# Kernel tuning notes

Hardware: AMD Instinct MI355X
Metric: run time of the kernel (lower is better)

Reference implementation:

```python
import jax, jax.numpy as jnp
import numpy as np

EPS = 1e-12
B, C, H, M, E, P = 2, 20000, 64, 8, 200000, 3


def setup_inputs() -> dict:
    key = jax.random.key(0)
    ks = jax.random.split(key, 24)
    inp = {}
    inp["features"] = jax.random.normal(ks[0], (B, C, H), jnp.float32)
    inp["positions"] = jax.random.normal(ks[1], (B, C, P), jnp.float32)
    inp["edge_index"] = jax.random.randint(ks[2], (2, E), 0, C)
    inp["degree"] = jax.random.randint(ks[3], (C,), 1, 33).astype(jnp.float32)
    inp["cell_node_indices"] = jax.random.randint(ks[4], (C, M), 0, C)
    mask = (jax.random.uniform(ks[5], (C, M)) > 0.3).astype(jnp.float32)
    inp["cell_node_mask"] = mask.at[:, 0].set(1.0)  # first node always valid (pad semantics)

    def lin(k, fan_in, fan_out):
        return (jax.random.normal(k, (fan_in, fan_out), jnp.float32) / np.sqrt(fan_in)).astype(jnp.float32)

    # message MLP: Linear(2H+4 -> H), SiLU, Linear(H -> H)
    inp["W1"] = lin(ks[6], 2 * H + 4, H); inp["b1"] = jnp.zeros((H,), jnp.float32)
    inp["W2"] = lin(ks[7], H, H);         inp["b2"] = jnp.zeros((H,), jnp.float32)
    # position MLP: Linear(H -> H), SiLU, Linear(H -> 1)
    inp["P1"] = lin(ks[8], H, H);  inp["pb1"] = jnp.zeros((H,), jnp.float32)
    inp["P2"] = lin(ks[9], H, 1);  inp["pb2"] = jnp.zeros((1,), jnp.float32)
    # update MLP: Linear(2H -> H), SiLU, Linear(H -> H)
    inp["U1"] = lin(ks[10], 2 * H, H); inp["ub1"] = jnp.zeros((H,), jnp.float32)
    inp["U2"] = lin(ks[11], H, H);     inp["ub2"] = jnp.zeros((H,), jnp.float32)
    return inp


def _mlp(x, Wa, ba, Wb, bb):
    return jax.nn.silu(x @ Wa + ba) @ Wb + bb


def _forward(features, positions, edge_index, degree, cell_node_indices, cell_node_mask,
             W1, b1, W2, b2, P1, pb1, P2, pb2, U1, ub1, U2, ub2):
    src, dst = edge_index[0], edge_index[1]
    # gather padded node positions per cell: [B, C, M, P]
    node_pos = positions[:, cell_node_indices]

    h_src = features[:, src]                      # [B,E,H]
    h_dst = features[:, dst]
    rel = positions[:, src] - positions[:, dst]   # [B,E,P]
    dist = jnp.linalg.norm(rel, axis=-1, keepdims=True)  # [B,E,1]

    sp = node_pos[:, src]                         # [B,E,M,P]
    dp = node_pos[:, dst]
    mx = cell_node_mask[src]                      # [E,M]
    my = cell_node_mask[dst]

    # pairwise distances [B,E,M,M] via gram trick (avoids [B,E,M,M,P] intermediate)
    sp2 = jnp.sum(sp * sp, -1)                    # [B,E,M]
    dp2 = jnp.sum(dp * dp, -1)
    cross = jnp.einsum('bemp,benp->bemn', sp, dp)
    d = jnp.sqrt(jnp.maximum(sp2[..., :, None] + dp2[..., None, :] - 2.0 * cross, 0.0) + EPS)

    # masked pairwise-distance sum
    w = mx[:, :, None] * my[:, None, :]           # [E,M,M]
    pairwise = jnp.sum(d * w[None], axis=(-1, -2))  # [B,E]

    # centroid distance
    denx = jnp.maximum(mx.sum(-1, keepdims=True), EPS)  # [E,1]
    deny = jnp.maximum(my.sum(-1, keepdims=True), EPS)
    cx = jnp.sum(sp * mx[None, :, :, None], axis=2) / denx[None]  # [B,E,P]
    cy = jnp.sum(dp * my[None, :, :, None], axis=2) / deny[None]
    centroid = jnp.linalg.norm(cx - cy, axis=-1)  # [B,E]

    # Hausdorff distance (masked min/max)
    inf = jnp.float32(jnp.inf)
    d_xy = jnp.where(my[None, :, None, :] <= 0, inf, d)
    min_xy = jnp.where(mx[None] <= 0, 0.0, d_xy.min(-1))  # [B,E,M]
    h_xy = min_xy.max(-1)                                  # [B,E]
    d_yx = jnp.where(mx[None, :, None, :] <= 0, inf, jnp.swapaxes(d, -1, -2))
    min_yx = jnp.where(my[None] <= 0, 0.0, d_yx.min(-1))
    h_yx = min_yx.max(-1)
    haus = jnp.maximum(h_xy, h_yx)

    invariants = jnp.concatenate([dist, pairwise[..., None], centroid[..., None], haus[..., None]], -1)  # [B,E,4]
    msg_in = jnp.concatenate([h_src, h_dst, invariants], -1)  # [B,E,2H+4]
    messages = _mlp(msg_in, W1, b1, W2, b2)                   # [B,E,H]

    # scatter-aggregate into destination cells, degree-normalize
    agg = jnp.zeros_like(features).at[:, dst].add(messages)
    agg = agg / jnp.maximum(degree, 1.0)[None, :, None]

    # position update
    wts = jnp.tanh(_mlp(messages, P1, pb1, P2, pb2))          # [B,E,1]
    pos_upd = jnp.zeros_like(positions).at[:, dst].add(wts * rel)

    new_features = features + _mlp(jnp.concatenate([features, agg], -1), U1, ub1, U2, ub2)
    new_positions = positions + pos_upd
    return new_features, new_positions


def reference(features, positions, edge_index, degree, cell_node_indices, cell_node_mask,
              W1, b1, W2, b2, P1, pb1, P2, pb2, U1, ub1, U2, ub2):
    return _forward(features, positions, edge_index, degree, cell_node_indices, cell_node_mask,
                    W1, b1, W2, b2, P1, pb1, P2, pb2, U1, ub1, U2, ub2)
```

## Files before the change

kernel.cpp:

```cpp
#include <hip/hip_runtime.h>
#include <hip/hip_bf16.h>

#define B_ 2
#define C_ 20000
#define H_ 64
#define M_ 8
#define E_ 200000
#define P_ 3
#define EPS_ 1e-12f
#define ET_ (E_ / 64)

typedef __attribute__((ext_vector_type(8))) short short8;
typedef __attribute__((ext_vector_type(4))) float float4v;

__device__ __forceinline__ float rcp_(float x)  { return __builtin_amdgcn_rcpf(x); }
__device__ __forceinline__ float sqrt_(float x) { return __builtin_amdgcn_sqrtf(x); }
__device__ __forceinline__ float silu_(float x) {
    return x * __builtin_amdgcn_rcpf(1.f + __expf(-x));
}
__device__ __forceinline__ float tanh_(float x) {
    float e = __expf(2.f * x);
    return 1.f - 2.f * __builtin_amdgcn_rcpf(e + 1.f);
}
__device__ __forceinline__ unsigned short f2b(float f) {
    unsigned u = __float_as_uint(f);
    unsigned r = (u + 0x7FFF + ((u >> 16) & 1)) >> 16;
    return (unsigned short)r;
}
__device__ __forceinline__ float b2f(unsigned short h) {
    return __uint_as_float(((unsigned)h) << 16);
}
__device__ __forceinline__ unsigned pk2u(float a, float b) {
    __hip_bfloat162 h = __float22bfloat162_rn(make_float2(a, b));
    unsigned u; __builtin_memcpy(&u, &h, sizeof(u)); return u;
}

#define W1S_OFF 0
#define W2S_OFF 8192
#define P1S_OFF 12288
#define U1S_OFF 16384
#define U2S_OFF 24576
#define WBUF_ELEMS 28672

#define NB_PREP  120
#define NB_FEATB 2500
#define NB_DESC  157
#define NB_HIST  782
#define NB_ZAGG  2500
#define NB_PCOPY 118
#define NB_COMBO (NB_PREP + NB_FEATB + NB_DESC + NB_HIST + NB_ZAGG + NB_PCOPY)

__global__ __launch_bounds__(256) void combo_kernel(
    const float* __restrict__ W1, const float* __restrict__ W2,
    const float* __restrict__ P1, const float* __restrict__ U1,
    const float* __restrict__ U2, unsigned short* __restrict__ wbuf,
    const float* __restrict__ feat, unsigned short* __restrict__ featb,
    const float* __restrict__ pos, const int* __restrict__ cni,
    const float* __restrict__ mask, float* __restrict__ desc,
    const int* __restrict__ ei, int* __restrict__ cnt,
    float* __restrict__ aggf, float* __restrict__ out_pos)
{
    const int bid = blockIdx.x;
    if (bid < NB_PREP) {
        int t = bid * 256 + threadIdx.x;
        if (t >= WBUF_ELEMS) return;
        const float* W; int e;
        if (t < W2S_OFF)      { W = W1; e = t; }
        else if (t < U1S_OFF) { W = (t < P1S_OFF) ? W2 : P1; e = (t < P1S_OFF) ? t - W2S_OFF : t - P1S_OFF; }
        else if (t < U2S_OFF) { W = U1; e = t - U1S_OFF; }
        else                  { W = U2; e = t - U2S_OFF; }
        int j = e & 7, lane = (e >> 3) & 63, nt = (e >> 9) & 3, kk = e >> 11;
        int k = kk * 32 + ((lane >> 4) * 8) + j;
        int n = nt * 16 + (lane & 15);
        wbuf[t] = f2b(W[k * 64 + n]);
    } else if (bid < NB_PREP + NB_FEATB) {
        int t = (bid - NB_PREP) * 256 + threadIdx.x;
        float4 v = *(const float4*)&feat[(size_t)t * 4];
        *(uint2*)&featb[(size_t)t * 4] = make_uint2(pk2u(v.x, v.y), pk2u(v.z, v.w));
    } else if (bid < NB_PREP + NB_FEATB + NB_DESC) {
        int tid = (bid - NB_PREP - NB_FEATB) * 256 + threadIdx.x;
        if (tid >= B_ * C_) return;
        int b = tid / C_, c = tid - b * C_;
        const float* pb = pos + (size_t)b * C_ * P_;
        float4* D = (float4*)(desc + (size_t)tid * 40);
        int4 n0 = *(const int4*)&cni[c*8];
        int4 n1 = *(const int4*)&cni[c*8 + 4];
        float4 m0 = *(const float4*)&mask[c*8];
        float4 m1 = *(const float4*)&mask[c*8 + 4];
        int ni[8] = {n0.x, n0.y, n0.z, n0.w, n1.x, n1.y, n1.z, n1.w};
        float mm[8] = {m0.x, m0.y, m0.z, m0.w, m1.x, m1.y, m1.z, m1.w};
        float sx = 0.f, sy = 0.f, sz = 0.f, sm = 0.f;
        #pragma unroll
        for (int m = 0; m < 8; ++m) {
            float x = pb[ni[m]*3+0], y = pb[ni[m]*3+1], z = pb[ni[m]*3+2];
            D[m] = make_float4(x, y, z, mm[m]);
            sx += x * mm[m]; sy += y * mm[m]; sz += z * mm[m]; sm += mm[m];
        }
        float inv = rcp_(fmaxf(sm, EPS_));
        D[8] = make_float4(sx * inv, sy * inv, sz * inv, sm);
        D[9] = make_float4(pb[c*3+0], pb[c*3+1], pb[c*3+2], 0.f);
    } else if (bid < NB_PREP + NB_FEATB + NB_DESC + NB_HIST) {
        int e = (bid - NB_PREP - NB_FEATB - NB_DESC) * 256 + threadIdx.x;
        if (e >= E_) return;
        atomicAdd(&cnt[ei[E_ + e]], 1);
    } else if (bid < NB_PREP + NB_FEATB + NB_DESC + NB_HIST + NB_ZAGG) {
        int t = (bid - NB_PREP - NB_FEATB - NB_DESC - NB_HIST) * 256 + threadIdx.x;
        *(float4*)&aggf[(size_t)t * 4] = make_float4(0.f, 0.f, 0.f, 0.f);
    } else {
        int t = (bid - NB_PREP - NB_FEATB - NB_DESC - NB_HIST - NB_ZAGG) * 256 + threadIdx.x;
        if (t >= (B_ * C_ * P_) / 4) return;
        *(float4*)&out_pos[(size_t)t * 4] = *(const float4*)&pos[(size_t)t * 4];
    }
}

__global__ __launch_bounds__(256) void alloc_kernel(
    const int* __restrict__ cnt, int* __restrict__ cursor, int* __restrict__ total)
{
    int idx = blockIdx.x * 256 + threadIdx.x;
    int lane = threadIdx.x & 63;
    int v = (idx < C_) ? cnt[idx] : 0;
    int inc = v;
    #pragma unroll
    for (int s = 1; s < 64; s <<= 1) {
        int n = __shfl_up(inc, s);
        if (lane >= s) inc += n;
    }
    int wtot = __shfl(inc, 63);
    int base = 0;
    if (lane == 0) base = atomicAdd(total, wtot);
    base = __shfl(base, 0);
    if (idx < C_) cursor[idx] = base + inc - v;
}

__global__ __launch_bounds__(256) void scatter_kernel(
    const int* __restrict__ ei, int* __restrict__ cursor, int2* __restrict__ sed)
{
    int e = blockIdx.x * 256 + threadIdx.x;
    if (e >= E_) return;
    int s = ei[e], d = ei[E_ + e];
    int slot = atomicAdd(&cursor[d], 1);
    sed[slot] = make_int2(s, d);
}

__global__ __launch_bounds__(256, 8) void edge_kernel(
    const unsigned short* __restrict__ featb,
    const int2* __restrict__ sed,
    const float* __restrict__ desc,
    const unsigned short* __restrict__ wbuf, const float* __restrict__ W1,
    const float* __restrict__ b1, const float* __restrict__ b2,
    const float* __restrict__ pb1, const float* __restrict__ P2,
    const float* __restrict__ pb2,
    float* __restrict__ aggf, float* __restrict__ out_pos)
{
    __shared__ unsigned short lds[4 * 2304];

    const int tid  = threadIdx.x;
    const int w    = tid >> 6;
    const int lane = tid & 63;
    const int q    = lane >> 4;
    const int l16  = lane & 15;
    const int w16  = w * 16;

    const int bidr = blockIdx.x;
    const int xcd  = bidr & 7, kblk = bidr >> 3;
    const int qq   = (B_ * ET_) >> 3, rr_ = (B_ * ET_) & 7;
    const int tile = (xcd < rr_ ? xcd * (qq + 1) : rr_ * (qq + 1) + (xcd - rr_) * qq) + kblk;

    const int b    = tile / ET_;
    const int i0   = (tile - b * ET_) * 64;
    const int2 sd  = sed[i0 + lane];
    const int s_l  = sd.x;
    const int d_l  = sd.y;
    const unsigned short* fb = featb + (size_t)b * C_ * H_;

    unsigned short* Xw = lds + w * 2304;
    unsigned short* Hw = Xw;
    unsigned short* Mw = Xw + 1152;

    const int sg = __shfl(s_l, w16 + l16);
    const int dg = __shfl(d_l, w16 + l16);
    const float4* Ds = (const float4*)(desc + ((size_t)b * C_ + sg) * 40);
    const float4* Dd = (const float4*)(desc + ((size_t)b * C_ + dg) * 40);

    float4 S[8];
    float rowmin[8];
    const float INFV = __builtin_inff();
    #pragma unroll
    for (int i = 0; i < 8; ++i) {
        S[i] = Ds[i];
        rowmin[i] = INFV;
    }
    float pair = 0.f, hyx = 0.f;
    #pragma unroll
    for (int jj = 0; jj < 2; ++jj) {
        float4 Dj = Dd[q*2 + jj];
        float colmin = INFV;
        #pragma unroll
        for (int i = 0; i < 8; ++i) {
            float dx = S[i].x - Dj.x, dy = S[i].y - Dj.y, dz = S[i].z - Dj.z;
            float dd = sqrt_(dx*dx + dy*dy + dz*dz + EPS_);
            pair += dd * S[i].w * Dj.w;
            rowmin[i] = (Dj.w  > 0.f) ? fminf(rowmin[i], dd) : rowmin[i];
            colmin    = (S[i].w > 0.f) ? fminf(colmin, dd)    : colmin;
        }
        hyx = fmaxf(hyx, (Dj.w > 0.f) ? colmin : 0.f);
    }
    pair += __shfl_xor(pair, 16);  pair += __shfl_xor(pair, 32);
    hyx = fmaxf(hyx, __shfl_xor(hyx, 16));  hyx = fmaxf(hyx, __shfl_xor(hyx, 32));
    #pragma unroll
    for (int i = 0; i < 8; ++i) {
        rowmin[i] = fminf(rowmin[i], __shfl_xor(rowmin[i], 16));
        rowmin[i] = fminf(rowmin[i], __shfl_xor(rowmin[i], 32));
    }
    float hxy = 0.f;
    #pragma unroll
    for (int i = 0; i < 8; ++i)
        hxy = fmaxf(hxy, (S[i].w > 0.f) ? rowmin[i] : 0.f);
    float4 Sc = Ds[8], Dc = Dd[8];
    float cdx = Sc.x - Dc.x, cdy = Sc.y - Dc.y, cdz = Sc.z - Dc.z;
    float4 Sp = Ds[9], Dp = Dd[9];
    const float relx = Sp.x - Dp.x, rely = Sp.y - Dp.y, relz = Sp.z - Dp.z;
    const float ivx = sqrt_(relx*relx + rely*rely + relz*relz);
    const float ivy = pair;
    const float ivz = sqrt_(cdx*cdx + cdy*cdy + cdz*cdz);
    const float ivw = fmaxf(hxy, hyx);

    const int rr4 = lane >> 4, c4 = lane & 15;
    #pragma unroll
    for (int it = 0; it < 4; ++it) {
        int rloc = it * 4 + rr4;
        int r = w16 + rloc;
        int sr = __shfl(s_l, r);
        int dr = __shfl(d_l, r);
        uint2 vs = *(const uint2*)&fb[(size_t)sr * 64 + c4 * 4];
        uint2 vd = *(const uint2*)&fb[(size_t)dr * 64 + c4 * 4];
        *(uint2*)&Xw[rloc*136 + c4*4]      = vs;
        *(uint2*)&Xw[rloc*136 + 64 + c4*4] = vd;
    }

    float4v acc[4];
    #pragma unroll
    for (int nt = 0; nt < 4; ++nt) {
        float bv = b1[nt*16 + l16];
        float wa = W1[128*64 + nt*16 + l16];
        float wb = W1[129*64 + nt*16 + l16];
        float wc = W1[130*64 + nt*16 + l16];
        float wd = W1[131*64 + nt*16 + l16];
        #pragma unroll
        for (int i = 0; i < 4; ++i) {
            int r = q*4 + i;
            acc[nt][i] = bv + __shfl(ivx, r)*wa + __shfl(ivy, r)*wb
                            + __shfl(ivz, r)*wc + __shfl(ivw, r)*wd;
        }
    }
    #pragma unroll
    for (int kk = 0; kk < 4; ++kk) {
        short8 a = *(const short8*)&Xw[l16*136 + kk*32 + q*8];
        #pragma unroll
        for (int nt = 0; nt < 4; ++nt) {
            short8 bf = *(const short8*)&wbuf[W1S_OFF + (((kk*4 + nt)*64) + lane) * 8];
            acc[nt] = __builtin_amdgcn_mfma_f32_16x16x32_bf16(a, bf, acc[nt], 0, 0, 0);
        }
    }
    #pragma unroll
    for (int nt = 0; nt < 4; ++nt)
        #pragma unroll
        for (int i = 0; i < 4; i += 2) {
            unsigned u = pk2u(silu_(acc[nt][i]), silu_(acc[nt][i+1]));
            Hw[(q*4 + i)*72     + nt*16 + l16] = (unsigned short)u;
            Hw[(q*4 + i + 1)*72 + nt*16 + l16] = (unsigned short)(u >> 16);
        }

    float4v mac[4];
    #pragma unroll
    for (int nt = 0; nt < 4; ++nt) {
        float bv = b2[nt*16 + l16];
        mac[nt] = (float4v){bv, bv, bv, bv};
    }
    #pragma unroll
    for (int kk = 0; kk < 2; ++kk) {
        short8 a = *(const short8*)&Hw[l16*72 + kk*32 + q*8];
        #pragma unroll
        for (int nt = 0; nt < 4; ++nt) {
            short8 bf = *(const short8*)&wbuf[W2S_OFF + (((kk*4 + nt)*64) + lane) * 8];
            mac[nt] = __builtin_amdgcn_mfma_f32_16x16x32_bf16(a, bf, mac[nt], 0, 0, 0);
        }
    }
    #pragma unroll
    for (int nt = 0; nt < 4; ++nt)
        #pragma unroll
        for (int i = 0; i < 4; i += 2) {
            unsigned u = pk2u(mac[nt][i], mac[nt][i+1]);
            Mw[(q*4 + i)*72     + nt*16 + l16] = (unsigned short)u;
            Mw[(q*4 + i + 1)*72 + nt*16 + l16] = (unsigned short)(u >> 16);
        }

    float4v gac[4];
    #pragma unroll
    for (int nt = 0; nt < 4; ++nt) {
        float bv = pb1[nt*16 + l16];
        gac[nt] = (float4v){bv, bv, bv, bv};
    }
    #pragma unroll
    for (int kk = 0; kk < 2; ++kk) {
        short8 a = *(const short8*)&Mw[l16*72 + kk*32 + q*8];
        #pragma unroll
        for (int nt = 0; nt < 4; ++nt) {
            short8 bf = *(const short8*)&wbuf[P1S_OFF + (((kk*4 + nt)*64) + lane) * 8];
            gac[nt] = __builtin_amdgcn_mfma_f32_16x16x32_bf16(a, bf, gac[nt], 0, 0, 0);
        }
    }
    float p2v[4];
    #pragma unroll
    for (int nt = 0; nt < 4; ++nt) p2v[nt] = P2[nt*16 + l16];
    const float pb2v = pb2[0];

    #pragma unroll
    for (int i = 0; i < 4; ++i) {
        float p = 0.f;
        #pragma unroll
        for (int nt = 0; nt < 4; ++nt) p += silu_(gac[nt][i]) * p2v[nt];
        p += __shfl_xor(p, 8);
        p += __shfl_xor(p, 4);
        p += __shfl_xor(p, 2);
        p += __shfl_xor(p, 1);
        float wt = tanh_(p + pb2v);
        if (l16 == 0) *(float*)&Mw[(q*4 + i)*72 + 64] = wt;
    }

    float mrow[16];
    #pragma unroll
    for (int rr = 0; rr < 16; ++rr) mrow[rr] = b2f(Mw[rr*72 + lane]);
    float wtl = *(const float*)&Mw[l16*72 + 64];

    float* aggB = aggf + (size_t)b * C_ * 64;
    float* opB  = out_pos + (size_t)b * C_ * 3;

    int dnext = __shfl(d_l, w16 + ((l16 + 1) & 15));
    bool bflag = (l16 == 15) || (dg != dnext);
    unsigned long long bal = __ballot(bflag);
    unsigned mask16 = __builtin_amdgcn_readfirstlane((unsigned)bal) & 0xFFFFu;

    unsigned below = mask16 & ((1u << l16) - 1u);
    int dist = l16 - (below ? (31 - __clz((int)below)) : -1) - 1;

    {
        float sx = wtl * relx, sy = wtl * rely, sz = wtl * relz;
        #pragma unroll
        for (int s = 1; s < 16; s <<= 1) {
            float tx = __shfl_up(sx, s);
            float ty = __shfl_up(sy, s);
            float tz = __shfl_up(sz, s);
            if (dist >= s) { sx += tx; sy += ty; sz += tz; }
        }
        if (bflag && q == 0) {
            float* p = &opB[(size_t)dg * 3];
            atomicAdd(p + 0, sx);
            atomicAdd(p + 1, sy);
            atomicAdd(p + 2, sz);
        }
    }

    float colacc = 0.f;
    #pragma unroll
    for (int rr = 0; rr < 16; ++rr) {
        colacc += mrow[rr];
        if (mask16 & (1u << rr)) {
            int dseg = __builtin_amdgcn_readlane(dg, rr);
            atomicAdd(&aggB[(size_t)dseg * 64 + lane], colacc);
            colacc = 0.f;
        }
    }
}

__global__ __launch_bounds__(256, 8) void node_kernel(
    const float* __restrict__ feat, const unsigned short* __restrict__ featb,
    const float* __restrict__ aggf, const float* __restrict__ deg,
    const unsigned short* __restrict__ wbuf,
    const float* __restrict__ ub1, const float* __restrict__ ub2,
    float* __restrict__ out_feat)
{
    __shared__ unsigned short lds[4 * 2304];

    const int tid  = threadIdx.x;
    const int w    = tid >> 6;
    const int lane = tid & 63;
    const int q    = lane >> 4;
    const int l16  = lane & 15;
    const int g0   = blockIdx.x * 64;

    unsigned short* Xw = lds + w * 2304;
    unsigned short* Hw = Xw;

    const int rr4 = lane >> 4, c4 = lane & 15;
    #pragma unroll
    for (int it = 0; it < 4; ++it) {
        int rloc = it * 4 + rr4;
        int g = g0 + w*16 + rloc;
        int gc = (g >= C_) ? g - C_ : g;
        float sc = rcp_(fmaxf(deg[gc], 1.f));
        uint2  vf = *(const uint2*)&featb[(size_t)g * 64 + c4 * 4];
        float4 va = *(const float4*)&aggf[(size_t)g * 64 + c4 * 4];
        *(uint2*)&Xw[rloc*136 + c4*4]      = vf;
        *(uint2*)&Xw[rloc*136 + 64 + c4*4] =
            make_uint2(pk2u(va.x*sc, va.y*sc), pk2u(va.z*sc, va.w*sc));
    }

    float4v acc[4];
    #pragma unroll
    for (int nt = 0; nt < 4; ++nt) {
        float bv = ub1[nt*16 + l16];
        acc[nt] = (float4v){bv, bv, bv, bv};
    }
    #pragma unroll
    for (int kk = 0; kk < 4; ++kk) {
        short8 a = *(const short8*)&Xw[l16*136 + kk*32 + q*8];
        #pragma unroll
        for (int nt = 0; nt < 4; ++nt) {
            short8 bf = *(const short8*)&wbuf[U1S_OFF + (((kk*4 + nt)*64) + lane) * 8];
            acc[nt] = __builtin_amdgcn_mfma_f32_16x16x32_bf16(a, bf, acc[nt], 0, 0, 0);
        }
    }
    #pragma unroll
    for (int nt = 0; nt < 4; ++nt)
        #pragma unroll
        for (int i = 0; i < 4; i += 2) {
            unsigned u = pk2u(silu_(acc[nt][i]), silu_(acc[nt][i+1]));
            Hw[(q*4 + i)*72     + nt*16 + l16] = (unsigned short)u;
            Hw[(q*4 + i + 1)*72 + nt*16 + l16] = (unsigned short)(u >> 16);
        }

    float4v oac[4];
    #pragma unroll
    for (int nt = 0; nt < 4; ++nt) {
        float bv = ub2[nt*16 + l16];
        oac[nt] = (float4v){bv, bv, bv, bv};
    }
    #pragma unroll
    for (int kk = 0; kk < 2; ++kk) {
        short8 a = *(const short8*)&Hw[l16*72 + kk*32 + q*8];
        #pragma unroll
        for (int nt = 0; nt < 4; ++nt) {
            short8 bf = *(const short8*)&wbuf[U2S_OFF + (((kk*4 + nt)*64) + lane) * 8];
            oac[nt] = __builtin_amdgcn_mfma_f32_16x16x32_bf16(a, bf, oac[nt], 0, 0, 0);
        }
    }
    #pragma unroll
    for (int nt = 0; nt < 4; ++nt)
        #pragma unroll
        for (int i = 0; i < 4; ++i) {
            size_t idx = (size_t)(g0 + w*16 + q*4 + i) * 64 + nt*16 + l16;
            out_feat[idx] = feat[idx] + oac[nt][i];
        }
}

extern "C" void kernel_launch(void* const* d_in, const int* in_sizes, int n_in,
                              void* d_out, int out_size, void* d_ws, size_t ws_size,
                              hipStream_t stream) {
    const float* feat = (const float*)d_in[0];
    const float* pos  = (const float*)d_in[1];
    const int*   ei   = (const int*)d_in[2];
    const float* deg  = (const float*)d_in[3];
    const int*   cni  = (const int*)d_in[4];
    const float* mask = (const float*)d_in[5];
    const float* W1   = (const float*)d_in[6];
    const float* b1   = (const float*)d_in[7];
    const float* W2   = (const float*)d_in[8];
    const float* b2   = (const float*)d_in[9];
    const float* P1   = (const float*)d_in[10];
    const float* pb1  = (const float*)d_in[11];
    const float* P2   = (const float*)d_in[12];
    const float* pb2  = (const float*)d_in[13];
    const float* U1   = (const float*)d_in[14];
    const float* ub1  = (const float*)d_in[15];
    const float* U2   = (const float*)d_in[16];
    const float* ub2  = (const float*)d_in[17];

    float* out_feat = (float*)d_out;
    float* out_pos  = out_feat + (size_t)B_ * C_ * H_;

    float* desc = (float*)d_ws;
    float* aggf = desc + (size_t)B_ * C_ * 40;
    unsigned short* featb = (unsigned short*)(aggf + (size_t)B_ * C_ * 64);
    unsigned short* wbuf  = featb + (size_t)B_ * C_ * 64;
    int* cnt    = (int*)(wbuf + WBUF_ELEMS);
    int* total  = cnt + C_;
    int* cursor = total + 1;
    int2* sed   = (int2*)(cursor + C_ + 1);

    hipMemsetAsync(cnt, 0, (C_ + 1) * sizeof(int), stream);

    combo_kernel<<<NB_COMBO, 256, 0, stream>>>(
        W1, W2, P1, U1, U2, wbuf, feat, featb, pos, cni, mask, desc, ei, cnt,
        aggf, out_pos);

    alloc_kernel<<<(C_ + 255) / 256, 256, 0, stream>>>(cnt, cursor, total);
    scatter_kernel<<<(E_ + 255) / 256, 256, 0, stream>>>(ei, cursor, sed);

    edge_kernel<<<B_ * ET_, 256, 0, stream>>>(
        featb, sed, desc, wbuf, W1, b1, b2, pb1, P2, pb2, aggf, out_pos);

    node_kernel<<<(B_ * C_) / 64, 256, 0, stream>>>(
        feat, featb, aggf, deg, wbuf, ub1, ub2, out_feat);
}
```

Before: 214.9 us.

## Move edge geometric invariants into scatter kernel, precompute per-slot

Computes the per-edge geometric invariants (distance, pairwise sum, centroid distance, Hausdorff) inside the scatter kernel, one thread per edge looping over batches. The results go to new workspace arrays indexed by the sorted slot. The edge kernel then reads four precomputed float4 values instead of gathering descriptors, running the 8x8 distance loop and doing cross-lane reductions. The aim is to take the geometry work out of the MFMA-heavy edge kernel and off its register budget. In exchange it adds extra global writes and reads of invariants and puts a serial 64-pair loop per thread into the scatter kernel, which has lower parallelism.

```diff
diff --git a/kernel.cpp b/kernel.cpp
--- a/kernel.cpp
+++ b/kernel.cpp
@@ -132,20 +132,59 @@
     if (idx < C_) cursor[idx] = base + inc - v;
 }
 
-__global__ __launch_bounds__(256) void scatter_kernel(
-    const int* __restrict__ ei, int* __restrict__ cursor, int2* __restrict__ sed)
+__global__ __launch_bounds__(256) void scatter_geom_kernel(
+    const int* __restrict__ ei, int* __restrict__ cursor,
+    const float* __restrict__ desc,
+    int2* __restrict__ sed, float4* __restrict__ ivA, float4* __restrict__ ivR)
 {
     int e = blockIdx.x * 256 + threadIdx.x;
     if (e >= E_) return;
     int s = ei[e], d = ei[E_ + e];
     int slot = atomicAdd(&cursor[d], 1);
     sed[slot] = make_int2(s, d);
+
+    const float INFV = __builtin_inff();
+    #pragma unroll 1
+    for (int b = 0; b < B_; ++b) {
+        const float4* Ds = (const float4*)(desc + ((size_t)b * C_ + s) * 40);
+        const float4* Dd = (const float4*)(desc + ((size_t)b * C_ + d) * 40);
+        float4 S[8]; float rowmin[8];
+        #pragma unroll
+        for (int i = 0; i < 8; ++i) { S[i] = Ds[i]; rowmin[i] = INFV; }
+        float pair = 0.f, hyx = 0.f;
+        #pragma unroll
+        for (int j = 0; j < 8; ++j) {
+            float4 Dj = Dd[j];
+            float colmin = INFV;
+            #pragma unroll
+            for (int i = 0; i < 8; ++i) {
+                float dx = S[i].x - Dj.x, dy = S[i].y - Dj.y, dz = S[i].z - Dj.z;
+                float dd = sqrt_(dx*dx + dy*dy + dz*dz + EPS_);
+                pair += dd * S[i].w * Dj.w;
+                rowmin[i] = (Dj.w  > 0.f) ? fminf(rowmin[i], dd) : rowmin[i];
+                colmin    = (S[i].w > 0.f) ? fminf(colmin, dd)   : colmin;
+            }
+            hyx = fmaxf(hyx, (Dj.w > 0.f) ? colmin : 0.f);
+        }
+        float hxy = 0.f;
+        #pragma unroll
+        for (int i = 0; i < 8; ++i)
+            hxy = fmaxf(hxy, (S[i].w > 0.f) ? rowmin[i] : 0.f);
+        float4 Sc = Ds[8], Dc = Dd[8];
+        float cdx = Sc.x - Dc.x, cdy = Sc.y - Dc.y, cdz = Sc.z - Dc.z;
+        float4 Sp = Ds[9], Dp = Dd[9];
+        float rx = Sp.x - Dp.x, ry = Sp.y - Dp.y, rz = Sp.z - Dp.z;
+        ivA[(size_t)b * E_ + slot] = make_float4(
+            sqrt_(rx*rx + ry*ry + rz*rz), pair,
+            sqrt_(cdx*cdx + cdy*cdy + cdz*cdz), fmaxf(hxy, hyx));
+        ivR[(size_t)b * E_ + slot] = make_float4(rx, ry, rz, 0.f);
+    }
 }
 
 __global__ __launch_bounds__(256, 8) void edge_kernel(
     const unsigned short* __restrict__ featb,
     const int2* __restrict__ sed,
-    const float* __restrict__ desc,
+    const float4* __restrict__ ivA, const float4* __restrict__ ivR,
     const unsigned short* __restrict__ wbuf, const float* __restrict__ W1,
     const float* __restrict__ b1, const float* __restrict__ b2,
     const float* __restrict__ pb1, const float* __restrict__ P2,
@@ -168,62 +207,22 @@
 
     const int b    = tile / ET_;
     const int i0   = (tile - b * ET_) * 64;
+    const unsigned short* fb = featb + (size_t)b * C_ * H_;
+
+    float4 iva[4];
+    #pragma unroll
+    for (int i = 0; i < 4; ++i)
+        iva[i] = ivA[(size_t)b * E_ + i0 + w16 + q*4 + i];
+    const float4 relv = ivR[(size_t)b * E_ + i0 + w16 + l16];
+
     const int2 sd  = sed[i0 + lane];
     const int s_l  = sd.x;
     const int d_l  = sd.y;
-    const unsigned short* fb = featb + (size_t)b * C_ * H_;
+    const int dg   = __shfl(d_l, w16 + l16);
 
     unsigned short* Xw = lds + w * 2304;
     unsigned short* Hw = Xw;
     unsigned short* Mw = Xw + 1152;
-
-    const int sg = __shfl(s_l, w16 + l16);
-    const int dg = __shfl(d_l, w16 + l16);
-    const float4* Ds = (const float4*)(desc + ((size_t)b * C_ + sg) * 40);
-    const float4* Dd = (const float4*)(desc + ((size_t)b * C_ + dg) * 40);
-
-    float4 S[8];
-    float rowmin[8];
-    const float INFV = __builtin_inff();
-    #pragma unroll
-    for (int i = 0; i < 8; ++i) {
-        S[i] = Ds[i];
-        rowmin[i] = INFV;
-    }
-    float pair = 0.f, hyx = 0.f;
-    #pragma unroll
-    for (int jj = 0; jj < 2; ++jj) {
-        float4 Dj = Dd[q*2 + jj];
-        float colmin = INFV;
-        #pragma unroll
-        for (int i = 0; i < 8; ++i) {
-            float dx = S[i].x - Dj.x, dy = S[i].y - Dj.y, dz = S[i].z - Dj.z;
-            float dd = sqrt_(dx*dx + dy*dy + dz*dz + EPS_);
-            pair += dd * S[i].w * Dj.w;
-            rowmin[i] = (Dj.w  > 0.f) ? fminf(rowmin[i], dd) : rowmin[i];
-            colmin    = (S[i].w > 0.f) ? fminf(colmin, dd)    : colmin;
-        }
-        hyx = fmaxf(hyx, (Dj.w > 0.f) ? colmin : 0.f);
-    }
-    pair += __shfl_xor(pair, 16);  pair += __shfl_xor(pair, 32);
-    hyx = fmaxf(hyx, __shfl_xor(hyx, 16));  hyx = fmaxf(hyx, __shfl_xor(hyx, 32));
-    #pragma unroll
-    for (int i = 0; i < 8; ++i) {
-        rowmin[i] = fminf(rowmin[i], __shfl_xor(rowmin[i], 16));
-        rowmin[i] = fminf(rowmin[i], __shfl_xor(rowmin[i], 32));
-    }
-    float hxy = 0.f;
-    #pragma unroll
-    for (int i = 0; i < 8; ++i)
-        hxy = fmaxf(hxy, (S[i].w > 0.f) ? rowmin[i] : 0.f);
-    float4 Sc = Ds[8], Dc = Dd[8];
-    float cdx = Sc.x - Dc.x, cdy = Sc.y - Dc.y, cdz = Sc.z - Dc.z;
-    float4 Sp = Ds[9], Dp = Dd[9];
-    const float relx = Sp.x - Dp.x, rely = Sp.y - Dp.y, relz = Sp.z - Dp.z;
-    const float ivx = sqrt_(relx*relx + rely*rely + relz*relz);
-    const float ivy = pair;
-    const float ivz = sqrt_(cdx*cdx + cdy*cdy + cdz*cdz);
-    const float ivw = fmaxf(hxy, hyx);
 
     const int rr4 = lane >> 4, c4 = lane & 15;
     #pragma unroll
@@ -247,11 +246,9 @@
         float wc = W1[130*64 + nt*16 + l16];
         float wd = W1[131*64 + nt*16 + l16];
         #pragma unroll
-        for (int i = 0; i < 4; ++i) {
-            int r = q*4 + i;
-            acc[nt][i] = bv + __shfl(ivx, r)*wa + __shfl(ivy, r)*wb
-                            + __shfl(ivz, r)*wc + __shfl(ivw, r)*wd;
-        }
+        for (int i = 0; i < 4; ++i)
+            acc[nt][i] = bv + iva[i].x*wa + iva[i].y*wb
+                            + iva[i].z*wc + iva[i].w*wd;
     }
     #pragma unroll
     for (int kk = 0; kk < 4; ++kk) {
@@ -345,7 +342,7 @@
     int dist = l16 - (below ? (31 - __clz((int)below)) : -1) - 1;
 
     {
-        float sx = wtl * relx, sy = wtl * rely, sz = wtl * relz;
+        float sx = wtl * relv.x, sy = wtl * relv.y, sz = wtl * relv.z;
         #pragma unroll
         for (int s = 1; s < 16; s <<= 1) {
             float tx = __shfl_up(sx, s);
@@ -479,9 +476,11 @@
     float* out_feat = (float*)d_out;
     float* out_pos  = out_feat + (size_t)B_ * C_ * H_;
 
-    float* desc = (float*)d_ws;
-    float* aggf = desc + (size_t)B_ * C_ * 40;
-    unsigned short* featb = (unsigned short*)(aggf + (size_t)B_ * C_ * 64);
+    float*  desc = (float*)d_ws;
+    float*  aggf = desc + (size_t)B_ * C_ * 40;
+    float4* ivA  = (float4*)(aggf + (size_t)B_ * C_ * 64);
+    float4* ivR  = ivA + (size_t)B_ * E_;
+    unsigned short* featb = (unsigned short*)(ivR + (size_t)B_ * E_);
     unsigned short* wbuf  = featb + (size_t)B_ * C_ * 64;
     int* cnt    = (int*)(wbuf + WBUF_ELEMS);
     int* total  = cnt + C_;
@@ -495,10 +494,12 @@
         aggf, out_pos);
 
     alloc_kernel<<<(C_ + 255) / 256, 256, 0, stream>>>(cnt, cursor, total);
-    scatter_kernel<<<(E_ + 255) / 256, 256, 0, stream>>>(ei, cursor, sed);
+
+    scatter_geom_kernel<<<(E_ + 255) / 256, 256, 0, stream>>>(
+        ei, cursor, desc, sed, ivA, ivR);
 
     edge_kernel<<<B_ * ET_, 256, 0, stream>>>(
-        featb, sed, desc, wbuf, W1, b1, b2, pb1, P2, pb2, aggf, out_pos);
+        featb, sed, ivA, ivR, wbuf, W1, b1, b2, pb1, P2, pb2, aggf, out_pos);
 
     node_kernel<<<(B_ * C_) / 64, 256, 0, stream>>>(
         feat, featb, aggf, deg, wbuf, ub1, ub2, out_feat);
```

Result: slower. 226.7 us (+5.5%).
